# Optimization experiments

Hardware: AMD Instinct MI355X
Metric: run time of the kernel (lower is better)

Reference implementation:

```python
import jax, jax.numpy as jnp
import numpy as np

B, S, VOCAB, D_MODEL, N_KERNELS, KSIZE, N_CLASSES = 8, 2048, 32000, 512, 256, 9, 4096
PAD = KSIZE // 2  # source uses kernel_size/2 (py2 int div)


def setup_inputs() -> dict:
    key = jax.random.key(0)
    ks = jax.random.split(key, 7)
    return {
        "text": jax.random.randint(ks[0], (B, S), 0, VOCAB),
        "embed_table": jax.random.normal(ks[1], (VOCAB, D_MODEL), dtype=jnp.float32) * 0.02,
        "conv_w": jax.random.normal(ks[2], (N_KERNELS, D_MODEL, KSIZE), dtype=jnp.float32) * 0.02,
        "conv_b": jax.random.normal(ks[3], (N_KERNELS,), dtype=jnp.float32) * 0.02,
        "U_w": jax.random.normal(ks[4], (N_CLASSES, N_KERNELS), dtype=jnp.float32) * 0.02,
        "final_w": jax.random.normal(ks[5], (N_CLASSES, N_KERNELS), dtype=jnp.float32) * 0.02,
        "final_b": jax.random.normal(ks[6], (N_CLASSES,), dtype=jnp.float32) * 0.02,
    }


def reference(text, embed_table, conv_w, conv_b, U_w, final_w, final_b):
    # Embedding lookup (tgt_embed); dropout is identity in eval mode.
    x = embed_table[text]                                  # [B, S, D]
    # Conv1d over sequence: NCH layout, OIH kernel, same-length padding.
    xc = jax.lax.conv_general_dilated(
        x.transpose(0, 2, 1), conv_w,
        window_strides=(1,), padding=[(PAD, PAD)],
        dimension_numbers=("NCH", "OIH", "NCH"))
    x = jnp.tanh(xc.transpose(0, 2, 1) + conv_b)           # [B, S, K]
    # Shared-query label attention: scores [B, n_classes, S].
    scores = jnp.einsum("ck,bsk->bcs", U_w, x)
    alpha = jax.nn.softmax(scores, axis=2)
    m = jnp.einsum("bcs,bsk->bck", alpha, x)               # [B, C, K]
    y = jnp.sum(final_w * m, axis=2) + final_b             # [B, C]
    return y
```

## Files before the change

### kernel.cpp

```cpp
#include <hip/hip_runtime.h>
#include <math.h>

#define B 8
#define S 2048
#define D_MODEL 512
#define NK 256
#define KSZ 9
#define NC 4096
#define PADW 4
#define SSPLIT 4
#define CM 64
#define CW (CM + 8)
#define NSTG (KSZ * 16)
#define NTILES ((S / SSPLIT) / 32)

typedef __attribute__((ext_vector_type(8))) short bf16x8;
typedef __attribute__((ext_vector_type(4))) float f32x4;

static __device__ __forceinline__ unsigned short f2bf(float f) {
    unsigned int u = __float_as_uint(f);
    unsigned int r = (u + 0x7fffu + ((u >> 16) & 1u)) >> 16;
    return (unsigned short)r;
}

#define GLOAD_LDS16(g, l) __builtin_amdgcn_global_load_lds( \
    (const __attribute__((address_space(1))) void*)(g),     \
    (__attribute__((address_space(3))) void*)(l), 16, 0, 0)

#define PREP_W (KSZ * NK * D_MODEL)
#define PREP_UF (NC * NK)
#define PREP_N (PREP_W + (2 * PREP_UF) / 4)
__global__ __launch_bounds__(256) void prep_all(
    const float* __restrict__ w, unsigned short* __restrict__ wtb,
    const float* __restrict__ U, unsigned short* __restrict__ Ub,
    const float* __restrict__ F, unsigned short* __restrict__ Fb)
{
    const float LOG2E = 1.44269504088896340736f;
    int idx = blockIdx.x * 256 + threadIdx.x;
    if (idx < PREP_W) {
        int dd  = idx & 31;
        int k   = (idx >> 5) & (NK - 1);
        int stg = idx >> 13;
        int t = stg >> 4, h = stg & 15;
        wtb[idx] = f2bf(w[((size_t)k * D_MODEL + h * 32 + dd) * KSZ + t]);
        return;
    }
    idx -= PREP_W;
    if (idx < PREP_UF / 4) {
        float4 v = ((const float4*)U)[idx];
        ushort4 o;
        o.x = f2bf(v.x * LOG2E); o.y = f2bf(v.y * LOG2E);
        o.z = f2bf(v.z * LOG2E); o.w = f2bf(v.w * LOG2E);
        ((ushort4*)Ub)[idx] = o;
        return;
    }
    idx -= PREP_UF / 4;
    if (idx < PREP_UF / 4) {
        float4 v = ((const float4*)F)[idx];
        ushort4 o;
        o.x = f2bf(v.x); o.y = f2bf(v.y);
        o.z = f2bf(v.z); o.w = f2bf(v.w);
        ((ushort4*)Fb)[idx] = o;
    }
}

__global__ __launch_bounds__(512, 2) void conv_mfma(
    const int* __restrict__ text, const float* __restrict__ emb,
    const unsigned short* __restrict__ wtb, const float* __restrict__ bias,
    unsigned short* __restrict__ xf)
{
    __shared__ unsigned short xs[CW * D_MODEL];
    const int b  = blockIdx.x >> 5;
    const int s0 = (blockIdx.x & 31) * CM;
    const int tid = threadIdx.x;

    for (int u = tid; u < CW * 64; u += 512) {
        int row = u >> 6, c = u & 63;
        int gs = s0 + row - PADW;
        float4 v0 = make_float4(0.f, 0.f, 0.f, 0.f), v1 = v0;
        if (gs >= 0 && gs < S) {
            int tok = text[b * S + gs];
            const float4* e4 = (const float4*)(emb + (size_t)tok * D_MODEL + c * 8);
            v0 = e4[0]; v1 = e4[1];
        }
        union { bf16x8 v; unsigned short us[8]; } pk;
        pk.us[0] = f2bf(v0.x); pk.us[1] = f2bf(v0.y);
        pk.us[2] = f2bf(v0.z); pk.us[3] = f2bf(v0.w);
        pk.us[4] = f2bf(v1.x); pk.us[5] = f2bf(v1.y);
        pk.us[6] = f2bf(v1.z); pk.us[7] = f2bf(v1.w);
        int phys = c ^ (row & 7);
        *(bf16x8*)(xs + row * D_MODEL + phys * 8) = pk.v;
    }
    __syncthreads();

    const int wv   = tid >> 6;
    const int lane = tid & 63;
    const int cl   = lane & 15;
    const int quad = lane >> 4;
    const int n0   = wv * 32;

    bf16x8 A0[4], A1[4], A2[4], B0[2], B1[2], B2[2];
    f32x4 acc[4][2] = {};

    #define LDB(BB, stg)                                                      \
        {                                                                     \
            const unsigned short* wp = wtb + (size_t)(stg) * (NK * 32)        \
                                       + (n0 + cl) * 32 + quad * 8;           \
            BB[0] = *(const bf16x8*)(wp);                                     \
            BB[1] = *(const bf16x8*)(wp + 16 * 32);                           \
        }
    #define LDA(AA, stg)                                                      \
        {                                                                     \
            int t_ = (stg) >> 4, h_ = (stg) & 15;                             \
            _Pragma("unroll")                                                 \
            for (int ms = 0; ms < 4; ms++) {                                  \
                int row = cl + ms * 16 + t_;                                  \
                int ph  = (h_ * 4 + quad) ^ (row & 7);                        \
                AA[ms] = *(const bf16x8*)(xs + row * D_MODEL + ph * 8);       \
            }                                                                 \
        }
    #define FENCE asm volatile("" ::: "memory");
    #define DOMFMA(AA, BB)                                                    \
        _Pragma("unroll")                                                     \
        for (int ms = 0; ms < 4; ms++) {                                      \
            acc[ms][0] = __builtin_amdgcn_mfma_f32_16x16x32_bf16(AA[ms], BB[0], acc[ms][0], 0, 0, 0); \
            acc[ms][1] = __builtin_amdgcn_mfma_f32_16x16x32_bf16(AA[ms], BB[1], acc[ms][1], 0, 0, 0); \
        }

    LDB(B0, 0) LDA(A0, 0) LDB(B1, 1) LDA(A1, 1) LDB(B2, 2) LDA(A2, 2) FENCE

    for (int ss = 0; ss < NSTG; ss += 3) {
        DOMFMA(A0, B0)
        if (ss + 3 < NSTG) { LDB(B0, ss + 3) LDA(A0, ss + 3) FENCE }
        DOMFMA(A1, B1)
        if (ss + 4 < NSTG) { LDB(B1, ss + 4) LDA(A1, ss + 4) FENCE }
        DOMFMA(A2, B2)
        if (ss + 5 < NSTG) { LDB(B2, ss + 5) LDA(A2, ss + 5) FENCE }
    }

    #pragma unroll
    for (int ns = 0; ns < 2; ns++) {
        const int k = n0 + ns * 16 + cl;
        const float bk = bias[k];
        #pragma unroll
        for (int ms = 0; ms < 4; ms++) {
            #pragma unroll
            for (int r = 0; r < 4; r++) {
                int s = s0 + ms * 16 + quad * 4 + r;
                float v = acc[ms][ns][r] + bk;
                float e = __expf(2.f * v);
                float th = 1.f - 2.f / (e + 1.f);
                xf[((size_t)b * S + s) * NK + k] = f2bf(th);
            }
        }
    }
}

__global__ __launch_bounds__(256, 2) void attn_mfma(
    const unsigned short* __restrict__ xf, const unsigned short* __restrict__ Ub,
    const unsigned short* __restrict__ Fb, float* __restrict__ pl,
    float* __restrict__ pg)
{
    __shared__ unsigned short xsa[2 * 32 * NK];
    const int b    = blockIdx.z;
    const int sp   = blockIdx.y;
    const int tid  = threadIdx.x;
    const int wv   = tid >> 6;
    const int lane = tid & 63;
    const int cl   = lane & 15;
    const int quad = lane >> 4;
    const int c0   = blockIdx.x * 128 + wv * 32;
    const int wvu  = __builtin_amdgcn_readfirstlane(wv);

    bf16x8 uf[2][8], ff[2][8];
    #pragma unroll
    for (int cg = 0; cg < 2; cg++) {
        const unsigned short* up = Ub + (size_t)(c0 + cg * 16 + cl) * NK + quad * 8;
        const unsigned short* fp = Fb + (size_t)(c0 + cg * 16 + cl) * NK + quad * 8;
        #pragma unroll
        for (int kk = 0; kk < 8; kk++) {
            uf[cg][kk] = *(const bf16x8*)(up + kk * 32);
            ff[cg][kk] = *(const bf16x8*)(fp + kk * 32);
        }
    }

    const int sbeg = sp * (S / SSPLIT);
    const unsigned short* xb = xf + ((size_t)b * S + sbeg) * NK;

    #define STAGE(bb, t)                                                      \
        {                                                                     \
            _Pragma("unroll")                                                 \
            for (int j = 0; j < 4; j++) {                                     \
                int C = j * 256 + tid;                                        \
                int r = C >> 5, p = C & 31;                                   \
                int jl = p ^ (r & 7);                                         \
                const unsigned short* src = xb + (size_t)((t) * 32 + r) * NK + jl * 8; \
                unsigned short* dst = xsa + (bb) * 8192 + j * 2048 + wvu * 512; \
                GLOAD_LDS16(src, dst);                                        \
            }                                                                 \
        }

    STAGE(0, 0)

    float l[2] = {0.f, 0.f}, G[2] = {0.f, 0.f};
    const int swz = cl & 7;

    for (int t = 0; t < NTILES; t++) {
        __syncthreads();
        if (t + 1 < NTILES) STAGE((t + 1) & 1, t + 1)

        const unsigned short* bs = xsa + (t & 1) * 8192;
        f32x4 sa[2][2] = {}, ga[2][2] = {};
        #pragma unroll
        for (int kk = 0; kk < 8; kk++) {
            int p0 = (quad + 4 * kk) ^ swz;
            bf16x8 a0 = *(const bf16x8*)(bs + cl * NK + p0 * 8);
            bf16x8 a1 = *(const bf16x8*)(bs + (16 + cl) * NK + p0 * 8);
            #pragma unroll
            for (int cg = 0; cg < 2; cg++) {
                sa[0][cg] = __builtin_amdgcn_mfma_f32_16x16x32_bf16(a0, uf[cg][kk], sa[0][cg], 0, 0, 0);
                ga[0][cg] = __builtin_amdgcn_mfma_f32_16x16x32_bf16(a0, ff[cg][kk], ga[0][cg], 0, 0, 0);
                sa[1][cg] = __builtin_amdgcn_mfma_f32_16x16x32_bf16(a1, uf[cg][kk], sa[1][cg], 0, 0, 0);
                ga[1][cg] = __builtin_amdgcn_mfma_f32_16x16x32_bf16(a1, ff[cg][kk], ga[1][cg], 0, 0, 0);
            }
        }

        #pragma unroll
        for (int cg = 0; cg < 2; cg++) {
            #pragma unroll
            for (int r = 0; r < 4; r++) {
                float e0 = exp2f(sa[0][cg][r]);
                float e1 = exp2f(sa[1][cg][r]);
                l[cg] += e0 + e1;
                G[cg] += e0 * ga[0][cg][r] + e1 * ga[1][cg][r];
            }
        }
    }

    #pragma unroll
    for (int cg = 0; cg < 2; cg++) {
        l[cg] += __shfl_xor(l[cg], 16); l[cg] += __shfl_xor(l[cg], 32);
        G[cg] += __shfl_xor(G[cg], 16); G[cg] += __shfl_xor(G[cg], 32);
    }
    if (lane < 16) {
        #pragma unroll
        for (int cg = 0; cg < 2; cg++) {
            size_t idx = ((size_t)b * SSPLIT + sp) * NC + c0 + cg * 16 + lane;
            pl[idx] = l[cg]; pg[idx] = G[cg];
        }
    }
}

__global__ __launch_bounds__(256) void combine_kernel(
    const float* __restrict__ pl, const float* __restrict__ pg,
    const float* __restrict__ fb, float* __restrict__ out)
{
    int idx = blockIdx.x * 256 + threadIdx.x;
    if (idx >= B * NC) return;
    int b = idx / NC, c = idx % NC;
    float l = 0.f, g = 0.f;
    #pragma unroll
    for (int sp = 0; sp < SSPLIT; sp++) {
        size_t i = ((size_t)b * SSPLIT + sp) * NC + c;
        l += pl[i];
        g += pg[i];
    }
    out[idx] = g / l + fb[c];
}

extern "C" void kernel_launch(void* const* d_in, const int* in_sizes, int n_in,
                              void* d_out, int out_size, void* d_ws, size_t ws_size,
                              hipStream_t stream) {
    const int*   text   = (const int*)  d_in[0];
    const float* emb    = (const float*)d_in[1];
    const float* conv_w = (const float*)d_in[2];
    const float* conv_b = (const float*)d_in[3];
    const float* U_w    = (const float*)d_in[4];
    const float* F_w    = (const float*)d_in[5];
    const float* f_b    = (const float*)d_in[6];
    float* out = (float*)d_out;

    char* ws = (char*)d_ws;
    unsigned short* xf  = (unsigned short*)ws; ws += (size_t)B * S * NK * 2;
    unsigned short* wtb = (unsigned short*)ws; ws += (size_t)KSZ * NK * D_MODEL * 2;
    unsigned short* Ub  = (unsigned short*)ws; ws += (size_t)NC * NK * 2;
    unsigned short* Fb  = (unsigned short*)ws; ws += (size_t)NC * NK * 2;
    float* pl = (float*)ws; ws += (size_t)SSPLIT * B * NC * 4;
    float* pg = (float*)ws; ws += (size_t)SSPLIT * B * NC * 4;

    prep_all<<<dim3((PREP_N + 255) / 256), 256, 0, stream>>>(conv_w, wtb, U_w, Ub, F_w, Fb);
    conv_mfma<<<dim3(B * S / CM), 512, 0, stream>>>(text, emb, wtb, conv_b, xf);
    attn_mfma<<<dim3(NC / 128, SSPLIT, B), 256, 0, stream>>>(xf, Ub, Fb, pl, pg);
    combine_kernel<<<dim3((B * NC + 255) / 256), 256, 0, stream>>>(pl, pg, f_b, out);
}
```

Before: 216.9 us.

## Load attention x tiles directly from global memory and remap blocks for XCD locality

Drops the LDS double-buffered staging of x tiles, which used global_load_lds plus a block-wide barrier per tile. Each wave now reads its A fragments straight from global memory, relying on L2/cache reuse across the four waves that share the same rows. The block index is also remapped so that consecutive hardware block ids spread across XCDs and blocks sharing a batch and sequence split land on the same XCD. This removes LDS traffic and barriers, at the cost of four times more global/L2 load requests per tile and less latency hiding.

```diff
diff --git a/kernel.cpp b/kernel.cpp
--- a/kernel.cpp
+++ b/kernel.cpp
@@ -23,10 +23,6 @@
     return (unsigned short)r;
 }
 
-#define GLOAD_LDS16(g, l) __builtin_amdgcn_global_load_lds( \
-    (const __attribute__((address_space(1))) void*)(g),     \
-    (__attribute__((address_space(3))) void*)(l), 16, 0, 0)
-
 #define PREP_W (KSZ * NK * D_MODEL)
 #define PREP_UF (NC * NK)
 #define PREP_N (PREP_W + (2 * PREP_UF) / 4)
@@ -161,16 +157,18 @@
     const unsigned short* __restrict__ Fb, float* __restrict__ pl,
     float* __restrict__ pg)
 {
-    __shared__ unsigned short xsa[2 * 32 * NK];
-    const int b    = blockIdx.z;
-    const int sp   = blockIdx.y;
+    int lin = blockIdx.x + 32 * (blockIdx.y + 4 * blockIdx.z);
+    int nid = (lin & 7) * 128 + (lin >> 3);
+    const int cblk = nid & 31;
+    const int sp   = (nid >> 5) & 3;
+    const int b    = nid >> 7;
+
     const int tid  = threadIdx.x;
     const int wv   = tid >> 6;
     const int lane = tid & 63;
     const int cl   = lane & 15;
     const int quad = lane >> 4;
-    const int c0   = blockIdx.x * 128 + wv * 32;
-    const int wvu  = __builtin_amdgcn_readfirstlane(wv);
+    const int c0   = cblk * 128 + wv * 32;
 
     bf16x8 uf[2][8], ff[2][8];
     #pragma unroll
@@ -185,37 +183,18 @@
     }
 
     const int sbeg = sp * (S / SSPLIT);
-    const unsigned short* xb = xf + ((size_t)b * S + sbeg) * NK;
-
-    #define STAGE(bb, t)                                                      \
-        {                                                                     \
-            _Pragma("unroll")                                                 \
-            for (int j = 0; j < 4; j++) {                                     \
-                int C = j * 256 + tid;                                        \
-                int r = C >> 5, p = C & 31;                                   \
-                int jl = p ^ (r & 7);                                         \
-                const unsigned short* src = xb + (size_t)((t) * 32 + r) * NK + jl * 8; \
-                unsigned short* dst = xsa + (bb) * 8192 + j * 2048 + wvu * 512; \
-                GLOAD_LDS16(src, dst);                                        \
-            }                                                                 \
-        }
-
-    STAGE(0, 0)
+    const unsigned short* xb = xf + ((size_t)b * S + sbeg) * NK
+                               + (size_t)cl * NK + quad * 8;
 
     float l[2] = {0.f, 0.f}, G[2] = {0.f, 0.f};
-    const int swz = cl & 7;
 
     for (int t = 0; t < NTILES; t++) {
-        __syncthreads();
-        if (t + 1 < NTILES) STAGE((t + 1) & 1, t + 1)
-
-        const unsigned short* bs = xsa + (t & 1) * 8192;
+        const unsigned short* ap = xb + (size_t)t * (32 * NK);
         f32x4 sa[2][2] = {}, ga[2][2] = {};
         #pragma unroll
         for (int kk = 0; kk < 8; kk++) {
-            int p0 = (quad + 4 * kk) ^ swz;
-            bf16x8 a0 = *(const bf16x8*)(bs + cl * NK + p0 * 8);
-            bf16x8 a1 = *(const bf16x8*)(bs + (16 + cl) * NK + p0 * 8);
+            bf16x8 a0 = *(const bf16x8*)(ap + kk * 32);
+            bf16x8 a1 = *(const bf16x8*)(ap + 16 * NK + kk * 32);
             #pragma unroll
             for (int cg = 0; cg < 2; cg++) {
                 sa[0][cg] = __builtin_amdgcn_mfma_f32_16x16x32_bf16(a0, uf[cg][kk], sa[0][cg], 0, 0, 0);
```

Result: slower. 282.9 us (+30.4%).

## Software-pipeline attention MFMA with softmax accumulation and remap block order

Applied to the files above, without the earlier changes.

The attention kernel now holds two sets of accumulators and overlaps the exp/accumulate step of one tile with the MFMA work of the next. This hides the transcendental and VALU latency behind matrix-core work. The block index is also remapped so that neighbouring launched blocks share a class-block stride pattern, probably for better cache or XCD locality. It also switches to the raw amdgcn exp2 intrinsic. In exchange, register pressure goes up under the 2-wave-per-SIMD launch bound.

```diff
diff --git a/kernel.cpp b/kernel.cpp
--- a/kernel.cpp
+++ b/kernel.cpp
@@ -162,14 +162,18 @@
     float* __restrict__ pg)
 {
     __shared__ unsigned short xsa[2 * 32 * NK];
-    const int b    = blockIdx.z;
-    const int sp   = blockIdx.y;
+    int lin = blockIdx.x + 32 * (blockIdx.y + 4 * blockIdx.z);
+    int nid = (lin & 7) * 128 + (lin >> 3);
+    const int cblk = nid & 31;
+    const int sp   = (nid >> 5) & 3;
+    const int b    = nid >> 7;
+
     const int tid  = threadIdx.x;
     const int wv   = tid >> 6;
     const int lane = tid & 63;
     const int cl   = lane & 15;
     const int quad = lane >> 4;
-    const int c0   = blockIdx.x * 128 + wv * 32;
+    const int c0   = cblk * 128 + wv * 32;
     const int wvu  = __builtin_amdgcn_readfirstlane(wv);
 
     bf16x8 uf[2][8], ff[2][8];
@@ -200,41 +204,64 @@
             }                                                                 \
         }
 
-    STAGE(0, 0)
-
     float l[2] = {0.f, 0.f}, G[2] = {0.f, 0.f};
     const int swz = cl & 7;
 
-    for (int t = 0; t < NTILES; t++) {
+    f32x4 saA[2][2], gaA[2][2], saB[2][2], gaB[2][2];
+
+    #define MFMAT(SA, GA, t)                                                  \
+    {                                                                         \
+        const unsigned short* bs = xsa + ((t) & 1) * 8192;                    \
+        _Pragma("unroll")                                                     \
+        for (int i = 0; i < 2; i++)                                           \
+            _Pragma("unroll")                                                 \
+            for (int j = 0; j < 2; j++) {                                     \
+                SA[i][j] = (f32x4){0.f, 0.f, 0.f, 0.f};                       \
+                GA[i][j] = (f32x4){0.f, 0.f, 0.f, 0.f};                       \
+            }                                                                 \
+        _Pragma("unroll")                                                     \
+        for (int kk = 0; kk < 8; kk++) {                                      \
+            int p0 = (quad + 4 * kk) ^ swz;                                   \
+            bf16x8 a0 = *(const bf16x8*)(bs + cl * NK + p0 * 8);              \
+            bf16x8 a1 = *(const bf16x8*)(bs + (16 + cl) * NK + p0 * 8);       \
+            _Pragma("unroll")                                                 \
+            for (int cg = 0; cg < 2; cg++) {                                  \
+                SA[0][cg] = __builtin_amdgcn_mfma_f32_16x16x32_bf16(a0, uf[cg][kk], SA[0][cg], 0, 0, 0); \
+                GA[0][cg] = __builtin_amdgcn_mfma_f32_16x16x32_bf16(a0, ff[cg][kk], GA[0][cg], 0, 0, 0); \
+                SA[1][cg] = __builtin_amdgcn_mfma_f32_16x16x32_bf16(a1, uf[cg][kk], SA[1][cg], 0, 0, 0); \
+                GA[1][cg] = __builtin_amdgcn_mfma_f32_16x16x32_bf16(a1, ff[cg][kk], GA[1][cg], 0, 0, 0); \
+            }                                                                 \
+        }                                                                     \
+    }
+
+    #define SMAX(SA, GA)                                                      \
+        _Pragma("unroll")                                                     \
+        for (int cg = 0; cg < 2; cg++) {                                      \
+            _Pragma("unroll")                                                 \
+            for (int r = 0; r < 4; r++) {                                     \
+                float e0 = __builtin_amdgcn_exp2f(SA[0][cg][r]);              \
+                float e1 = __builtin_amdgcn_exp2f(SA[1][cg][r]);              \
+                l[cg] += e0 + e1;                                             \
+                G[cg] += e0 * GA[0][cg][r] + e1 * GA[1][cg][r];               \
+            }                                                                 \
+        }
+
+    STAGE(0, 0)
+    __syncthreads();
+    STAGE(1, 1)
+    MFMAT(saA, gaA, 0)
+
+    for (int tp = 1; tp < NTILES; tp += 2) {
         __syncthreads();
-        if (t + 1 < NTILES) STAGE((t + 1) & 1, t + 1)
-
-        const unsigned short* bs = xsa + (t & 1) * 8192;
-        f32x4 sa[2][2] = {}, ga[2][2] = {};
-        #pragma unroll
-        for (int kk = 0; kk < 8; kk++) {
-            int p0 = (quad + 4 * kk) ^ swz;
-            bf16x8 a0 = *(const bf16x8*)(bs + cl * NK + p0 * 8);
-            bf16x8 a1 = *(const bf16x8*)(bs + (16 + cl) * NK + p0 * 8);
-            #pragma unroll
-            for (int cg = 0; cg < 2; cg++) {
-                sa[0][cg] = __builtin_amdgcn_mfma_f32_16x16x32_bf16(a0, uf[cg][kk], sa[0][cg], 0, 0, 0);
-                ga[0][cg] = __builtin_amdgcn_mfma_f32_16x16x32_bf16(a0, ff[cg][kk], ga[0][cg], 0, 0, 0);
-                sa[1][cg] = __builtin_amdgcn_mfma_f32_16x16x32_bf16(a1, uf[cg][kk], sa[1][cg], 0, 0, 0);
-                ga[1][cg] = __builtin_amdgcn_mfma_f32_16x16x32_bf16(a1, ff[cg][kk], ga[1][cg], 0, 0, 0);
-            }
-        }
-
-        #pragma unroll
-        for (int cg = 0; cg < 2; cg++) {
-            #pragma unroll
-            for (int r = 0; r < 4; r++) {
-                float e0 = exp2f(sa[0][cg][r]);
-                float e1 = exp2f(sa[1][cg][r]);
-                l[cg] += e0 + e1;
-                G[cg] += e0 * ga[0][cg][r] + e1 * ga[1][cg][r];
-            }
-        }
+        if (tp + 1 < NTILES) STAGE((tp + 1) & 1, tp + 1)
+        MFMAT(saB, gaB, tp)
+        SMAX(saA, gaA)
+        if (tp + 1 < NTILES) {
+            __syncthreads();
+            if (tp + 2 < NTILES) STAGE((tp + 2) & 1, tp + 2)
+            MFMAT(saA, gaA, tp + 1)
+        }
+        SMAX(saB, gaB)
     }
 
     #pragma unroll
```

New measurement: 228.1 us. +5.2%, slower.
